# Performance work log

Measured on AMD Instinct MI355X. Metric: run time of the kernel, lower is better.

The kernel has to match this reference:

```python
import jax, jax.numpy as jnp
import numpy as np

B, N, ND, ED = 4, 24, 13, 12          # batch, num_nodes, node feat dim, edge feat dim
H, NH, HD = 256, 8, 32                # hidden, heads, head dim (H == NH*HD)
L, T = 64, 1000                       # transformer layers, max_timestep
_SCALE = 1.0 / float(np.sqrt(H))      # torch divides by sqrt(node_dim)=sqrt(256)


def _ln(x, g, b):
    m = x.mean(-1, keepdims=True)
    v = ((x - m) ** 2).mean(-1, keepdims=True)
    return (x - m) / jnp.sqrt(v + 1e-5) * g + b


def setup_inputs() -> dict:
    key = jax.random.key(0)
    it = iter(jax.random.split(key, 40))
    def w(*s):
        return (jax.random.normal(next(it), s) * 0.02).astype(jnp.float32)
    z = lambda *s: jnp.zeros(s, jnp.float32)
    o = lambda *s: jnp.ones(s, jnp.float32)
    d = {}
    d['nodes'] = jax.random.normal(next(it), (B, N, ND), jnp.float32)
    d['edges'] = jax.random.normal(next(it), (B, N, N, ED), jnp.float32)
    d['conds'] = jax.random.randint(next(it), (B,), 0, T)
    # input MLPs
    d['inN_w1'] = w(ND, H); d['inN_b1'] = z(H); d['inN_w2'] = w(H, H); d['inN_b2'] = z(H)
    d['inE_w1'] = w(ED, H); d['inE_b1'] = z(H); d['inE_w2'] = w(H, H); d['inE_b2'] = z(H)
    d['inC_w1'] = w(T, H);  d['inC_b1'] = z(H); d['inC_w2'] = w(H, H); d['inC_b2'] = z(H)
    # stacked per-layer params (leading dim L, scanned)
    d['qkv_w'] = w(L, H, 3 * H); d['qkv_b'] = z(L, 3 * H)
    d['no_w'] = w(L, H, H); d['no_b'] = z(L, H)
    d['eo_w'] = w(L, H, H); d['eo_b'] = z(L, H)
    d['ln1n_g'] = o(L, H); d['ln1n_b'] = z(L, H)
    d['ln1e_g'] = o(L, H); d['ln1e_b'] = z(L, H)
    d['mn_w1'] = w(L, H, 4 * H); d['mn_b1'] = z(L, 4 * H)
    d['mn_w2'] = w(L, 4 * H, H); d['mn_b2'] = z(L, H)
    d['me_w1'] = w(L, H, 4 * H); d['me_b1'] = z(L, 4 * H)
    d['me_w2'] = w(L, 4 * H, H); d['me_b2'] = z(L, H)
    d['ln2n_g'] = o(L, H); d['ln2n_b'] = z(L, H)
    d['ln2e_g'] = o(L, H); d['ln2e_b'] = z(L, H)
    # output MLPs
    d['outN_w1'] = w(H, H); d['outN_b1'] = z(H); d['outN_w2'] = w(H, ND); d['outN_b2'] = z(ND)
    d['outE_w1'] = w(H, H); d['outE_b1'] = z(H); d['outE_w2'] = w(H, ED); d['outE_b2'] = z(ED)
    return d


def _forward(nodes, edges, conds,
             inN_w1, inN_b1, inN_w2, inN_b2, inE_w1, inE_b1, inE_w2, inE_b2,
             inC_w1, inC_b1, inC_w2, inC_b2,
             qkv_w, qkv_b, no_w, no_b, eo_w, eo_b,
             ln1n_g, ln1n_b, ln1e_g, ln1e_b,
             mn_w1, mn_b1, mn_w2, mn_b2, me_w1, me_b1, me_w2, me_b2,
             ln2n_g, ln2n_b, ln2e_g, ln2e_b,
             outN_w1, outN_b1, outN_w2, outN_b2, outE_w1, outE_b1, outE_w2, outE_b2):
    relu = jax.nn.relu
    c = jax.nn.one_hot(conds, T, dtype=nodes.dtype)
    c = relu(relu(c @ inC_w1 + inC_b1) @ inC_w2 + inC_b2)          # (B,H)
    n = relu(relu(nodes @ inN_w1 + inN_b1) @ inN_w2 + inN_b2)      # (B,N,H)
    e = relu(relu(edges @ inE_w1 + inE_b1) @ inE_w2 + inE_b2)      # (B,N,N,H)

    def layer(carry, p):
        n, e = carry
        (qw, qb, nw, nb, ew, eb, g1n, b1n, g1e, b1e,
         w1n, bb1n, w2n, bb2n, w1e, bb1e, w2e, bb2e, g2n, b2n, g2e, b2e) = p
        nc = n + c[:, None, :]
        q, k, v = jnp.split(nc @ qw + qb, 3, axis=-1)
        q = q.reshape(B, N, NH, HD); k = k.reshape(B, N, NH, HD); v = v.reshape(B, N, NH, HD)
        s5 = jnp.einsum('bihd,bjhd->bijhd', q, k) * _SCALE          # (B,N,N,NH,HD)
        ne5 = s5 + e.reshape(B, N, N, NH, HD)                       # edge-biased scores
        attn = jax.nn.softmax(ne5.sum(-1), axis=2)                  # (B,N,N,NH)
        wv = jnp.einsum('bijh,bjhd->bihd', attn, v).reshape(B, N, H)
        an = _ln(wv @ nw + nb + n, g1n, b1n)
        ae = _ln(relu(ne5.reshape(B, N, N, H) @ ew + eb) + e, g1e, b1e)
        n2 = _ln(relu(an @ w1n + bb1n) @ w2n + bb2n + an, g2n, b2n)
        e2 = _ln(relu(ae @ w1e + bb1e) @ w2e + bb2e + ae, g2e, b2e)
        return (n2, e2), None

    stacked = (qkv_w, qkv_b, no_w, no_b, eo_w, eo_b, ln1n_g, ln1n_b, ln1e_g, ln1e_b,
               mn_w1, mn_b1, mn_w2, mn_b2, me_w1, me_b1, me_w2, me_b2,
               ln2n_g, ln2n_b, ln2e_g, ln2e_b)
    (n, e), _ = jax.lax.scan(layer, (n, e), stacked)
    out_n = relu(n @ outN_w1 + outN_b1) @ outN_w2 + outN_b2
    out_e = relu(e @ outE_w1 + outE_b1) @ outE_w2 + outE_b2
    return out_n, out_e


def reference(nodes, edges, conds,
              inN_w1, inN_b1, inN_w2, inN_b2, inE_w1, inE_b1, inE_w2, inE_b2,
              inC_w1, inC_b1, inC_w2, inC_b2,
              qkv_w, qkv_b, no_w, no_b, eo_w, eo_b,
              ln1n_g, ln1n_b, ln1e_g, ln1e_b,
              mn_w1, mn_b1, mn_w2, mn_b2, me_w1, me_b1, me_w2, me_b2,
              ln2n_g, ln2n_b, ln2e_g, ln2e_b,
              outN_w1, outN_b1, outN_w2, outN_b2, outE_w1, outE_b1, outE_w2, outE_b2):
    return _forward(nodes, edges, conds,
                    inN_w1, inN_b1, inN_w2, inN_b2, inE_w1, inE_b1, inE_w2, inE_b2,
                    inC_w1, inC_b1, inC_w2, inC_b2,
                    qkv_w, qkv_b, no_w, no_b, eo_w, eo_b,
                    ln1n_g, ln1n_b, ln1e_g, ln1e_b,
                    mn_w1, mn_b1, mn_w2, mn_b2, me_w1, me_b1, me_w2, me_b2,
                    ln2n_g, ln2n_b, ln2e_g, ln2e_b,
                    outN_w1, outN_b1, outN_w2, outN_b2, outE_w1, outE_b1, outE_w2, outE_b2)
```

## Files before the change

### kernel.cpp

```cpp
#include <hip/hip_runtime.h>

typedef _Float16 half_t;
typedef _Float16 f16x8 __attribute__((ext_vector_type(8)));
typedef _Float16 f16x4 __attribute__((ext_vector_type(4)));
typedef float f32x4 __attribute__((ext_vector_type(4)));

#define BB 4
#define NNODE 24
#define NLAYER 64
#define SCALE_QK 0.0625f

#define WS_C     0
#define WS_N     1024
#define WS_NACC  25600
#define NACC_STRIDE 24576
#define WS_E     74752
#define WS_AE32  664576
#define WS_AE16  1254400
#define WS_AN16  1549312
#define WS_EPART 1561600
#define EPART_SLICE 589824
#define WS_WTF   3920896
#define SLOT_F16 1376256
#define OFF_QKVT 0
#define OFF_NOT  196608
#define OFF_EOT  262144
#define OFF_MN1T 327680
#define OFF_MN2T 589824
#define OFF_ME1T 851968
#define OFF_ME2T 1114112
#define OFF_INE2T  (3*SLOT_F16)
#define OFF_OUTE1T (3*SLOT_F16 + 65536)

struct Params {
  const float *nodes, *edges; const int* conds;
  const float *inN_w1,*inN_b1,*inN_w2,*inN_b2;
  const float *inE_w1,*inE_b1,*inE_w2,*inE_b2;
  const float *inC_w1,*inC_b1,*inC_w2,*inC_b2;
  const float *qkv_w,*qkv_b,*no_w,*no_b,*eo_w,*eo_b;
  const float *ln1n_g,*ln1n_b,*ln1e_g,*ln1e_b;
  const float *mn_w1,*mn_b1,*mn_w2,*mn_b2,*me_w1,*me_b1,*me_w2,*me_b2;
  const float *ln2n_g,*ln2n_b,*ln2e_g,*ln2e_b;
  const float *outN_w1,*outN_b1,*outN_w2,*outN_b2,*outE_w1,*outE_b1,*outE_w2,*outE_b2;
  float* ws; float* out;
};

template<int NT, int KS, int MT, int LDAH>
__device__ __forceinline__ void gemm_rs_acc(const half_t* __restrict__ WT, int ldb,
                                            const char* __restrict__ A,
                                            f32x4 (&acc)[NT][MT]) {
  const int lane = threadIdx.x & 63;
  const int wv = threadIdx.x >> 6;
  const int l15 = lane & 15;
  const int kg = lane >> 4;
  f16x8 b[NT][KS];
#pragma unroll
  for (int nt = 0; nt < NT; ++nt) {
    const int col = (nt * 8 + wv) * 16 + l15;
#pragma unroll
    for (int ks = 0; ks < KS; ++ks)
      b[nt][ks] = *(const f16x8*)(WT + (size_t)col * ldb + ks * 32 + kg * 8);
  }
#pragma unroll
  for (int m = 0; m < MT; ++m) {
    f16x8 a[KS];
    const int row = m * 16 + l15;
#pragma unroll
    for (int ks = 0; ks < KS; ++ks)
      a[ks] = *(const f16x8*)(A + row * (LDAH * 2) + (((ks * 32 + kg * 8) * 2) ^ ((row & 7) << 4)));
#pragma unroll
    for (int ks = 0; ks < KS; ++ks)
#pragma unroll
      for (int nt = 0; nt < NT; ++nt)
        acc[nt][m] = __builtin_amdgcn_mfma_f32_16x16x32_f16(a[ks], b[nt][ks], acc[nt][m], 0, 0, 0);
  }
}

template<int NT, int KS, int MT, int LDAH, typename EPI>
__device__ __forceinline__ void gemm_rs(const half_t* __restrict__ WT, int ldb,
                                        const char* __restrict__ A, EPI epi) {
  f32x4 acc[NT][MT];
#pragma unroll
  for (int nt = 0; nt < NT; ++nt)
#pragma unroll
    for (int m = 0; m < MT; ++m) {
      f32x4 z = {0.f, 0.f, 0.f, 0.f};
      acc[nt][m] = z;
    }
  gemm_rs_acc<NT, KS, MT, LDAH>(WT, ldb, A, acc);
#pragma unroll
  for (int nt = 0; nt < NT; ++nt)
#pragma unroll
    for (int m = 0; m < MT; ++m)
      epi(nt, m, acc[nt][m]);
}

template<int NTW, int KT, int MT, int LDA, int LDB, typename EPI>
__device__ __forceinline__ void run_gemm_s(const half_t* __restrict__ WT,
                                           const char* __restrict__ A,
                                           EPI epi) {
  const int lane = threadIdx.x & 63;
  const int wv = threadIdx.x >> 6;
  const int l15 = lane & 15;
  const int kg = lane >> 4;
  constexpr int NC = KT / 8;
  constexpr int TC = NC * NTW;
  f16x8 bb[2][8];
  auto ldb = [&](int c, int w) {
    const int kc = c / NTW, n = c % NTW;
    const half_t* bp = WT + (size_t)((n * 8 + wv) * 16 + l15) * LDB + kc * 256 + kg * 8;
#pragma unroll
    for (int q = 0; q < 8; ++q) bb[w][q] = *(const f16x8*)(bp + q * 32);
  };
  f32x4 acc[NTW][MT];
#pragma unroll
  for (int n = 0; n < NTW; ++n)
#pragma unroll
    for (int m = 0; m < MT; ++m) {
      f32x4 z = {0.f, 0.f, 0.f, 0.f};
      acc[n][m] = z;
    }
  ldb(0, 0);
#pragma unroll
  for (int kc = 0; kc < NC; ++kc) {
    f16x8 a[8][MT];
#pragma unroll
    for (int q = 0; q < 8; ++q) {
      const int k0 = (kc * 8 + q) * 32 + kg * 8;
#pragma unroll
      for (int m = 0; m < MT; ++m) {
        const int row = m * 16 + l15;
        a[q][m] = *(const f16x8*)(A + row * (LDA * 2) + ((k0 * 2) ^ ((row & 7) << 4)));
      }
    }
#pragma unroll
    for (int n = 0; n < NTW; ++n) {
      const int c = kc * NTW + n;
      if (c + 1 < TC) ldb(c + 1, (c + 1) & 1);
#pragma unroll
      for (int q = 0; q < 8; ++q)
#pragma unroll
        for (int m = 0; m < MT; ++m)
          acc[n][m] = __builtin_amdgcn_mfma_f32_16x16x32_f16(a[q][m], bb[c & 1][q], acc[n][m], 0, 0, 0);
    }
  }
#pragma unroll
  for (int n = 0; n < NTW; ++n) epi(n, acc[n]);
}

__device__ void conv_matrix_tile(const float* __restrict__ src, half_t* __restrict__ dst,
                                 int K, int Nn, int tk, int tn, char* smem) {
  float* tl = (float*)smem;
  const int t = threadIdx.x;
  const int c = t & 63;
  const int r0 = t >> 6;
  for (int r = r0; r < 64; r += 8)
    tl[r * 65 + c] = src[(size_t)(tk * 64 + r) * Nn + tn * 64 + c];
  __syncthreads();
  for (int r = r0; r < 64; r += 8)
    dst[(size_t)(tn * 64 + r) * K + tk * 64 + c] = (half_t)tl[c * 65 + r];
  __syncthreads();
}

__device__ void conv_layer_tile(const Params& p, half_t* slot, int lw, int tile, char* smem) {
  if (tile < 48)       { conv_matrix_tile(p.qkv_w + (size_t)lw*196608, slot+OFF_QKVT, 256, 768, tile & 3, tile >> 2, smem); }
  else if (tile < 64)  { int t2 = tile-48;  conv_matrix_tile(p.no_w  + (size_t)lw*65536,  slot+OFF_NOT,  256, 256, t2 & 3,  t2 >> 2, smem); }
  else if (tile < 80)  { int t2 = tile-64;  conv_matrix_tile(p.eo_w  + (size_t)lw*65536,  slot+OFF_EOT,  256, 256, t2 & 3,  t2 >> 2, smem); }
  else if (tile < 144) { int t2 = tile-80;  conv_matrix_tile(p.mn_w1 + (size_t)lw*262144, slot+OFF_MN1T, 256, 1024, t2 & 3, t2 >> 2, smem); }
  else if (tile < 208) { int t2 = tile-144; conv_matrix_tile(p.mn_w2 + (size_t)lw*262144, slot+OFF_MN2T, 1024, 256, t2 & 15, t2 >> 4, smem); }
  else if (tile < 272) { int t2 = tile-208; conv_matrix_tile(p.me_w1 + (size_t)lw*262144, slot+OFF_ME1T, 256, 1024, t2 & 3, t2 >> 2, smem); }
  else                 { int t2 = tile-272; conv_matrix_tile(p.me_w2 + (size_t)lw*262144, slot+OFF_ME2T, 1024, 256, t2 & 15, t2 >> 4, smem); }
}

__global__ __launch_bounds__(512, 2) void k_embedA(Params p) {
  __shared__ __align__(16) char smem[17024];
  const int bid = blockIdx.x, tid = threadIdx.x;
  float* ws = p.ws;
  half_t* wt = (half_t*)(ws + WS_WTF);
  if (bid < 4) {
    const int b = bid;
    const int cond = p.conds[b];
    float* t1 = (float*)smem;
    if (tid < 256) t1[tid] = fmaxf(p.inC_w1[(size_t)cond * 256 + tid] + p.inC_b1[tid], 0.f);
    __syncthreads();
    if (tid < 256) {
      float s = p.inC_b2[tid];
      for (int k = 0; k < 256; ++k) s += t1[k] * p.inC_w2[(size_t)k * 256 + tid];
      ws[WS_C + b * 256 + tid] = fmaxf(s, 0.f);
    }
  } else {
    for (int job = bid - 4; job < 704; job += 128) {
      if (job < 336)      conv_layer_tile(p, wt, 0, job, smem);
      else if (job < 672) conv_layer_tile(p, wt + SLOT_F16, 1, job - 336, smem);
      else if (job < 688) { int t2 = job - 672; conv_matrix_tile(p.inE_w2,  wt + OFF_INE2T,  256, 256, t2 & 3, t2 >> 2, smem); }
      else                { int t2 = job - 688; conv_matrix_tile(p.outE_w1, wt + OFF_OUTE1T, 256, 256, t2 & 3, t2 >> 2, smem); }
    }
  }
}

__global__ __launch_bounds__(512, 2) void k_embedB(Params p) {
  __shared__ __align__(16) char smem[24640];
  const int bid = blockIdx.x, tid = threadIdx.x;
  const int lane = tid & 63, wv = tid >> 6, l15 = lane & 15, kg = lane >> 4;
  float* ws = p.ws;
  half_t* wt = (half_t*)(ws + WS_WTF);
  float* e0 = ws + WS_E;
  float* n0 = ws + WS_N;
  if (bid < 96) {
    const int b = bid / NNODE, i = bid % NNODE;
    float* eb = (float*)smem;
    char* t16 = smem + 2048;
    for (int idx = tid; idx < 24 * 12; idx += 512)
      eb[idx] = p.edges[((size_t)(b * NNODE + i) * NNODE + idx / 12) * 12 + idx % 12];
    __syncthreads();
    for (int idx = tid; idx < 32 * 32; idx += 512) {
      int r = idx >> 5, kb = idx & 31, k0 = kb * 8;
      f16x8 v;
#pragma unroll
      for (int j = 0; j < 8; ++j) v[j] = (half_t)0.f;
      if (r < NNODE) {
#pragma unroll
        for (int j = 0; j < 8; ++j) {
          int col = k0 + j;
          float s = p.inE_b1[col];
          for (int kk = 0; kk < 12; ++kk) s += eb[r * 12 + kk] * p.inE_w1[kk * 256 + col];
          v[j] = (half_t)fmaxf(s, 0.f);
        }
      }
      *(f16x8*)(t16 + r * 512 + ((k0 * 2) ^ ((r & 7) << 4))) = v;
    }
    __syncthreads();
    run_gemm_s<2, 8, 2, 256, 256>(wt + OFF_INE2T, t16,
      [&](int n, f32x4 (&accn)[2]) {
        const int col = (n * 8 + wv) * 16 + l15;
        const float bcol = p.inE_b2[col];
#pragma unroll
        for (int m = 0; m < 2; ++m)
#pragma unroll
          for (int r4 = 0; r4 < 4; ++r4) {
            const int row = m * 16 + kg * 4 + r4;
            if (row < NNODE)
              e0[((size_t)(b * NNODE + i) * NNODE + row) * 256 + col] = fmaxf(accn[m][r4] + bcol, 0.f);
          }
      });
  } else {
    const int nb = bid - 96, b = nb >> 1, hf = nb & 1, i0 = hf * 12;
    float* nd = (float*)smem;
    float* t1 = (float*)(smem + 1024);
    for (int idx = tid; idx < 12 * 13; idx += 512)
      nd[(idx / 13) * 16 + (idx % 13)] = p.nodes[(size_t)(b * NNODE + i0 + idx / 13) * 13 + idx % 13];
    __syncthreads();
    for (int idx = tid; idx < 12 * 256; idx += 512) {
      int r = idx >> 8, col = idx & 255;
      float s = p.inN_b1[col];
      for (int kk = 0; kk < 13; ++kk) s += nd[r * 16 + kk] * p.inN_w1[kk * 256 + col];
      t1[r * 257 + col] = fmaxf(s, 0.f);
    }
    __syncthreads();
    {
      int col = tid & 255, rh = tid >> 8;
      float a6[6] = {0.f, 0.f, 0.f, 0.f, 0.f, 0.f};
      for (int k = 0; k < 256; ++k) {
        float w = p.inN_w2[(size_t)k * 256 + col];
#pragma unroll
        for (int r = 0; r < 6; ++r) a6[r] += t1[(rh * 6 + r) * 257 + k] * w;
      }
#pragma unroll
      for (int r = 0; r < 6; ++r) {
        int row = rh * 6 + r;
        n0[(size_t)(b * NNODE + i0 + row) * 256 + col] = fmaxf(a6[r] + p.inN_b2[col], 0.f);
      }
    }
  }
}

__global__ __launch_bounds__(512, 2) void k_attn(Params p, int lyr) {
  __shared__ __align__(16) char smem[139488];
  const int bid = blockIdx.x, tid = threadIdx.x;
  const int lane = tid & 63, wv = tid >> 6, l15 = lane & 15, kg = lane >> 4;
  float* ws = p.ws;
  half_t* wt = (half_t*)(ws + WS_WTF);
  const half_t* slot = wt + (size_t)(lyr % 3) * SLOT_F16;

  if (bid >= 96) {
    if (lyr + 2 < NLAYER) {
      half_t* dslot = wt + (size_t)((lyr + 2) % 3) * SLOT_F16;
      for (int tile = bid - 96; tile < 336; tile += 126)
        conv_layer_tile(p, dslot, lyr + 2, tile, smem);
    }
    return;
  }
  const int b = bid / NNODE, i = bid % NNODE;
  const size_t rowbase = (size_t)(b * NNODE + i) * NNODE;
  char* nc16 = smem;
  half_t* qkv16 = (half_t*)(smem + 16384);
  char* ne5 = smem + 65536;
  float* e32 = (float*)(smem + 81920);
  float* psum = (float*)(smem + 106880);
  float* sc = (float*)(smem + 109952);
  float* wvl = (float*)(smem + 110720);
  float* ni = (float*)(smem + 111744);
  float* anr = (float*)(smem + 112768);
  float* aef = (float*)(smem + 114816);
  float* ae32 = ws + WS_AE32;
  half_t* ae16g = (half_t*)(ws + WS_AE16);
  const half_t* epart = (const half_t*)(ws + WS_EPART);
  const float* nacc_in = ws + WS_NACC + ((lyr + 1) & 1) * NACC_STRIDE;
  float* nacc_out = ws + WS_NACC + (lyr & 1) * NACC_STRIDE;
  const float* cb = ws + WS_C + b * 256;

  for (int r = wv; r < 32; r += 8) {
    const int c = lane * 4;
    f16x4 hv;
    if (r < NNODE) {
      f32x4 y;
      if (lyr == 0) {
        y = *(const f32x4*)(ws + WS_N + (size_t)(b * NNODE + r) * 256 + c);
      } else {
        f32x4 x = *(const f32x4*)(nacc_in + (size_t)(b * NNODE + r) * 256 + c);
        float s = x[0] + x[1] + x[2] + x[3];
        float s2 = x[0]*x[0] + x[1]*x[1] + x[2]*x[2] + x[3]*x[3];
#pragma unroll
        for (int off = 32; off; off >>= 1) { s += __shfl_xor(s, off); s2 += __shfl_xor(s2, off); }
        float mean = s * (1.f / 256.f);
        float rstd = rsqrtf(s2 * (1.f / 256.f) - mean * mean + 1e-5f);
        const float* g = p.ln2n_g + (size_t)(lyr - 1) * 256;
        const float* bv = p.ln2n_b + (size_t)(lyr - 1) * 256;
#pragma unroll
        for (int j = 0; j < 4; ++j) y[j] = (x[j] - mean) * rstd * g[c + j] + bv[c + j];
      }
      if (r == i) *(f32x4*)(ni + c) = y;
#pragma unroll
      for (int j = 0; j < 4; ++j) hv[j] = (half_t)(y[j] + cb[c + j]);
    } else {
#pragma unroll
      for (int j = 0; j < 4; ++j) hv[j] = (half_t)0.f;
    }
    *(f16x4*)(nc16 + r * 512 + ((lane * 8) ^ ((r & 7) << 4))) = hv;
  }
  __syncthreads();
  {
    const float* qb = p.qkv_b + (size_t)lyr * 768;
#pragma unroll
    for (int nn = 0; nn < 3; ++nn) {
      gemm_rs<2, 8, 2, 256>(slot + OFF_QKVT + (size_t)(nn * 256) * 256, 256, nc16,
        [&](int nt, int m, f32x4 v) {
          const int gcol = nn * 256 + (nt * 8 + wv) * 16 + l15;
          const float bc = qb[gcol];
#pragma unroll
          for (int r4 = 0; r4 < 4; ++r4) {
            const int row = m * 16 + kg * 4 + r4;
            qkv16[(size_t)row * 768 + gcol] = (half_t)(v[r4] + bc);
          }
        });
    }
  }
  __syncthreads();
  for (int idx = tid; idx < 32 * 32; idx += 512) {
    int r = idx >> 5, kb = idx & 31, k0 = kb * 8;
    f16x8 v;
#pragma unroll
    for (int j = 0; j < 8; ++j) v[j] = (half_t)0.f;
    if (r < NNODE) {
      const size_t row = rowbase + r;
      float x[8];
      if (lyr == 0) {
        const f32x4 a = *(const f32x4*)(ws + WS_E + row * 256 + k0);
        const f32x4 b4 = *(const f32x4*)(ws + WS_E + row * 256 + k0 + 4);
#pragma unroll
        for (int j = 0; j < 4; ++j) { x[j] = a[j]; x[4 + j] = b4[j]; }
      } else {
        const float* mb2 = p.me_b2 + (size_t)(lyr - 1) * 256;
        const f32x4 a = *(const f32x4*)(ae32 + row * 256 + k0);
        const f32x4 b4 = *(const f32x4*)(ae32 + row * 256 + k0 + 4);
#pragma unroll
        for (int j = 0; j < 4; ++j) { x[j] = a[j] + mb2[k0 + j]; x[4 + j] = b4[j] + mb2[k0 + 4 + j]; }
#pragma unroll
        for (int hb = 0; hb < 8; ++hb) {
          f16x8 pv = *(const f16x8*)(epart + (size_t)hb * EPART_SLICE + row * 256 + k0);
#pragma unroll
          for (int j = 0; j < 8; ++j) x[j] += (float)pv[j];
        }
        float s = 0.f, s2 = 0.f;
#pragma unroll
        for (int j = 0; j < 8; ++j) { s += x[j]; s2 += x[j] * x[j]; }
#pragma unroll
        for (int off = 16; off; off >>= 1) { s += __shfl_xor(s, off); s2 += __shfl_xor(s2, off); }
        float mean = s * (1.f / 256.f);
        float rstd = rsqrtf(s2 * (1.f / 256.f) - mean * mean + 1e-5f);
        const float* g = p.ln2e_g + (size_t)(lyr - 1) * 256;
        const float* bv = p.ln2e_b + (size_t)(lyr - 1) * 256;
#pragma unroll
        for (int j = 0; j < 8; ++j) x[j] = (x[j] - mean) * rstd * g[k0 + j] + bv[k0 + j];
      }
      f16x8 q8 = *(const f16x8*)(qkv16 + (size_t)i * 768 + k0);
      f16x8 k8 = *(const f16x8*)(qkv16 + (size_t)r * 768 + 256 + k0);
      float ps = 0.f;
#pragma unroll
      for (int j = 0; j < 8; ++j) {
        float f = SCALE_QK * (float)q8[j] * (float)k8[j] + x[j];
        v[j] = (half_t)f;
        ps += f;
        e32[r * 260 + k0 + j] = x[j];
      }
      psum[r * 32 + kb] = ps;
    }
    *(f16x8*)(ne5 + r * 512 + ((k0 * 2) ^ ((r & 7) << 4))) = v;
  }
  __syncthreads();
  if (tid < 192) {
    int hq = tid & 7;
    sc[tid] = psum[(tid >> 3) * 32 + hq * 4] + psum[(tid >> 3) * 32 + hq * 4 + 1] +
              psum[(tid >> 3) * 32 + hq * 4 + 2] + psum[(tid >> 3) * 32 + hq * 4 + 3];
  }
  __syncthreads();
  if (tid < 8) {
    const int h = tid;
    float mx = -1e30f;
#pragma unroll
    for (int j = 0; j < 24; ++j) mx = fmaxf(mx, sc[j * 8 + h]);
    float ex[24]; float ssum = 0.f;
#pragma unroll
    for (int j = 0; j < 24; ++j) { ex[j] = __expf(sc[j * 8 + h] - mx); ssum += ex[j]; }
    float inv = 1.f / ssum;
#pragma unroll
    for (int j = 0; j < 24; ++j) sc[j * 8 + h] = ex[j] * inv;
  }
  __syncthreads();
  if (tid < 256) {
    const int d = tid, h = d >> 5;
    float a = 0.f;
#pragma unroll
    for (int j = 0; j < 24; ++j) a += sc[j * 8 + h] * (float)qkv16[(size_t)j * 768 + 512 + d];
    wvl[d] = a;
  }
  {
    const float* eob = p.eo_b + (size_t)lyr * 256;
    gemm_rs<2, 8, 2, 256>(slot + OFF_EOT, 256, ne5,
      [&](int nt, int m, f32x4 v) {
        const int col = (nt * 8 + wv) * 16 + l15;
#pragma unroll
        for (int r4 = 0; r4 < 4; ++r4) {
          const int row = m * 16 + kg * 4 + r4;
          if (row < NNODE)
            aef[row * 257 + col] = fmaxf(v[r4] + eob[col], 0.f) + e32[row * 260 + col];
        }
      });
  }
  __syncthreads();
  {
    const float* g = p.ln1e_g + (size_t)lyr * 256;
    const float* bv = p.ln1e_b + (size_t)lyr * 256;
    for (int r = wv; r < NNODE; r += 8) {
      float x[4];
#pragma unroll
      for (int j = 0; j < 4; ++j) x[j] = aef[r * 257 + lane * 4 + j];
      float s = x[0] + x[1] + x[2] + x[3];
      float s2 = x[0]*x[0] + x[1]*x[1] + x[2]*x[2] + x[3]*x[3];
#pragma unroll
      for (int off = 32; off; off >>= 1) { s += __shfl_xor(s, off); s2 += __shfl_xor(s2, off); }
      float mean = s * (1.f / 256.f);
      float rstd = rsqrtf(s2 * (1.f / 256.f) - mean * mean + 1e-5f);
      f16x4 hv; f32x4 yv;
#pragma unroll
      for (int j = 0; j < 4; ++j) {
        int c = lane * 4 + j;
        float y = (x[j] - mean) * rstd * g[c] + bv[c];
        yv[j] = y; hv[j] = (half_t)y;
      }
      *(f32x4*)(ae32 + (rowbase + r) * 256 + lane * 4) = yv;
      *(f16x4*)(ae16g + (rowbase + r) * 256 + lane * 4) = hv;
    }
  }
  {
    const half_t* NOT_ = slot + OFF_NOT;
    int c = tid & 255, hf = tid >> 8;
    float s = 0.f;
    const half_t* wp = NOT_ + (size_t)c * 256 + hf * 128;
#pragma unroll
    for (int k8 = 0; k8 < 16; ++k8) {
      f16x8 w8 = *(const f16x8*)(wp + k8 * 8);
#pragma unroll
      for (int j = 0; j < 8; ++j) s += wvl[hf * 128 + k8 * 8 + j] * (float)w8[j];
    }
    anr[hf * 256 + c] = s;
  }
  __syncthreads();
  if (wv == 0) {
    const float* nob = p.no_b + (size_t)lyr * 256;
    const float* g = p.ln1n_g + (size_t)lyr * 256;
    const float* bv = p.ln1n_b + (size_t)lyr * 256;
    const float* mb2 = p.mn_b2 + (size_t)lyr * 256;
    float x[4];
#pragma unroll
    for (int j = 0; j < 4; ++j) {
      int c = lane * 4 + j;
      x[j] = anr[c] + anr[256 + c] + nob[c] + ni[c];
    }
    float s = x[0] + x[1] + x[2] + x[3];
    float s2 = x[0]*x[0] + x[1]*x[1] + x[2]*x[2] + x[3]*x[3];
#pragma unroll
    for (int off = 32; off; off >>= 1) { s += __shfl_xor(s, off); s2 += __shfl_xor(s2, off); }
    float mean = s * (1.f / 256.f);
    float rstd = rsqrtf(s2 * (1.f / 256.f) - mean * mean + 1e-5f);
    f16x4 hv; f32x4 av;
#pragma unroll
    for (int j = 0; j < 4; ++j) {
      int c = lane * 4 + j;
      float y = (x[j] - mean) * rstd * g[c] + bv[c];
      hv[j] = (half_t)y;
      av[j] = y + mb2[c];
    }
    *(f16x4*)((half_t*)(ws + WS_AN16) + (size_t)(b * NNODE + i) * 256 + lane * 4) = hv;
    *(f32x4*)(nacc_out + (size_t)(b * NNODE + i) * 256 + lane * 4) = av;
  }
}

__global__ __launch_bounds__(512, 2) void k_mlp(Params p, int lyr) {
  __shared__ __align__(16) char smem[73728];
  const int bid = blockIdx.x, tid = threadIdx.x;
  const int lane = tid & 63, wv = tid >> 6, l15 = lane & 15, kg = lane >> 4;
  float* ws = p.ws;
  half_t* wt = (half_t*)(ws + WS_WTF);
  const half_t* slot = wt + (size_t)(lyr % 3) * SLOT_F16;

  if (bid < 192) {
    const int rb = bid >> 3, hb = bid & 7;
    const int row0 = rb * 96;
    char* A16 = smem;
    char* hl = smem + 49152;
    const half_t* aeg = (const half_t*)(ws + WS_AE16) + (size_t)row0 * 256;
    for (int idx = tid; idx < 96 * 32; idx += 512) {
      int r = idx >> 5, c8 = idx & 31;
      f16x8 v = *(const f16x8*)(aeg + r * 256 + c8 * 8);
      *(f16x8*)(A16 + r * 512 + ((c8 * 16) ^ ((r & 7) << 4))) = v;
    }
    __syncthreads();
    const float* mb1 = p.me_b1 + (size_t)lyr * 1024 + hb * 128;
    gemm_rs<1, 8, 6, 256>(slot + OFF_ME1T + (size_t)(hb * 128) * 256, 256, A16,
      [&](int nt, int m, f32x4 v) {
        const int colb = wv * 16 + l15;
        const float bc = mb1[colb];
#pragma unroll
        for (int r4 = 0; r4 < 4; ++r4) {
          const int row = m * 16 + kg * 4 + r4;
          *(half_t*)(hl + row * 256 + ((colb * 2) ^ ((row & 7) << 4))) = (half_t)fmaxf(v[r4] + bc, 0.f);
        }
      });
    __syncthreads();
    half_t* ep = (half_t*)(ws + WS_EPART) + (size_t)hb * EPART_SLICE + (size_t)row0 * 256;
    gemm_rs<2, 4, 6, 128>(slot + OFF_ME2T + hb * 128, 1024, hl,
      [&](int nt, int m, f32x4 v) {
        const int col = (nt * 8 + wv) * 16 + l15;
#pragma unroll
        for (int r4 = 0; r4 < 4; ++r4)
          ep[(size_t)(m * 16 + kg * 4 + r4) * 256 + col] = (half_t)v[r4];
      });
  } else {
    const int hb = bid - 192;
    char* A16 = smem;
    char* hl = smem + 49152;
    const half_t* ang = (const half_t*)(ws + WS_AN16);
    for (int idx = tid; idx < 96 * 32; idx += 512) {
      int r = idx >> 5, c8 = idx & 31;
      f16x8 v = *(const f16x8*)(ang + (size_t)r * 256 + c8 * 8);
      *(f16x8*)(A16 + r * 512 + ((c8 * 16) ^ ((r & 7) << 4))) = v;
    }
    __syncthreads();
    const float* mb1 = p.mn_b1 + (size_t)lyr * 1024 + hb * 128;
    gemm_rs<1, 8, 6, 256>(slot + OFF_MN1T + (size_t)(hb * 128) * 256, 256, A16,
      [&](int nt, int m, f32x4 v) {
        const int colb = wv * 16 + l15;
        const float bc = mb1[colb];
#pragma unroll
        for (int r4 = 0; r4 < 4; ++r4) {
          const int row = m * 16 + kg * 4 + r4;
          *(half_t*)(hl + row * 256 + ((colb * 2) ^ ((row & 7) << 4))) = (half_t)fmaxf(v[r4] + bc, 0.f);
        }
      });
    __syncthreads();
    float* nacc_out = ws + WS_NACC + (lyr & 1) * NACC_STRIDE;
    gemm_rs<2, 4, 6, 128>(slot + OFF_MN2T + hb * 128, 1024, hl,
      [&](int nt, int m, f32x4 v) {
        const int col = (nt * 8 + wv) * 16 + l15;
#pragma unroll
        for (int r4 = 0; r4 < 4; ++r4)
          atomicAdd(&nacc_out[(size_t)(m * 16 + kg * 4 + r4) * 256 + col], v[r4]);
      });
  }
}

__global__ __launch_bounds__(512, 2) void k_out(Params p) {
  __shared__ __align__(16) char smem[49472];
  const int bid = blockIdx.x, tid = threadIdx.x;
  const int lane = tid & 63, wv = tid >> 6, l15 = lane & 15, kg = lane >> 4;
  float* ws = p.ws;
  half_t* wt = (half_t*)(ws + WS_WTF);
  const float* ae32 = ws + WS_AE32;
  const half_t* epart = (const half_t*)(ws + WS_EPART);
  if (bid < 96) {
    const int b = bid / NNODE, i = bid % NNODE;
    const size_t rowbase = (size_t)(b * NNODE + i) * NNODE;
    char* A16 = smem;
    float* h2f = (float*)(smem + 16384);
    const float* mb2 = p.me_b2 + (size_t)63 * 256;
    const float* g = p.ln2e_g + (size_t)63 * 256;
    const float* bvv = p.ln2e_b + (size_t)63 * 256;
    for (int idx = tid; idx < 32 * 32; idx += 512) {
      int r = idx >> 5, kb = idx & 31, k0 = kb * 8;
      f16x8 v;
#pragma unroll
      for (int j = 0; j < 8; ++j) v[j] = (half_t)0.f;
      if (r < NNODE) {
        const size_t row = rowbase + r;
        float x[8];
        const f32x4 a = *(const f32x4*)(ae32 + row * 256 + k0);
        const f32x4 b4 = *(const f32x4*)(ae32 + row * 256 + k0 + 4);
#pragma unroll
        for (int j = 0; j < 4; ++j) { x[j] = a[j] + mb2[k0 + j]; x[4 + j] = b4[j] + mb2[k0 + 4 + j]; }
#pragma unroll
        for (int hb = 0; hb < 8; ++hb) {
          f16x8 pv = *(const f16x8*)(epart + (size_t)hb * EPART_SLICE + row * 256 + k0);
#pragma unroll
          for (int j = 0; j < 8; ++j) x[j] += (float)pv[j];
        }
        float s = 0.f, s2 = 0.f;
#pragma unroll
        for (int j = 0; j < 8; ++j) { s += x[j]; s2 += x[j] * x[j]; }
#pragma unroll
        for (int off = 16; off; off >>= 1) { s += __shfl_xor(s, off); s2 += __shfl_xor(s2, off); }
        float mean = s * (1.f / 256.f);
        float rstd = rsqrtf(s2 * (1.f / 256.f) - mean * mean + 1e-5f);
#pragma unroll
        for (int j = 0; j < 8; ++j)
          v[j] = (half_t)((x[j] - mean) * rstd * g[k0 + j] + bvv[k0 + j]);
      }
      *(f16x8*)(A16 + r * 512 + ((k0 * 2) ^ ((r & 7) << 4))) = v;
    }
    __syncthreads();
    run_gemm_s<2, 8, 2, 256, 256>(wt + OFF_OUTE1T, A16,
      [&](int n, f32x4 (&accn)[2]) {
        const int col = (n * 8 + wv) * 16 + l15;
#pragma unroll
        for (int m = 0; m < 2; ++m)
#pragma unroll
          for (int r4 = 0; r4 < 4; ++r4) {
            const int row = m * 16 + kg * 4 + r4;
            h2f[row * 257 + col] = (row < NNODE) ? fmaxf(accn[m][r4] + p.outE_b1[col], 0.f) : 0.f;
          }
      });
    __syncthreads();
    for (int pr = tid; pr < 24 * 12; pr += 512) {
      int j = pr / 12, oc = pr % 12;
      float s = p.outE_b2[oc];
      for (int k = 0; k < 256; ++k) s += h2f[j * 257 + k] * p.outE_w2[k * 12 + oc];
      p.out[1248 + ((size_t)(b * NNODE + i) * NNODE + j) * 12 + oc] = s;
    }
  } else {
    const int nb = bid - 96, bq = nb >> 1, hf = nb & 1, i0 = hf * 12;
    float* nl = (float*)smem;
    float* t1f = (float*)(smem + 12544);
    const float* n_acc = ws + WS_NACC + 1 * NACC_STRIDE;
    const float* g = p.ln2n_g + (size_t)63 * 256;
    const float* bvv = p.ln2n_b + (size_t)63 * 256;
    for (int r = wv; r < 12; r += 8) {
      const int row = bq * NNODE + i0 + r;
      const int c = lane * 4;
      f32x4 x = *(const f32x4*)(n_acc + (size_t)row * 256 + c);
      float s = x[0] + x[1] + x[2] + x[3];
      float s2 = x[0]*x[0] + x[1]*x[1] + x[2]*x[2] + x[3]*x[3];
#pragma unroll
      for (int off = 32; off; off >>= 1) { s += __shfl_xor(s, off); s2 += __shfl_xor(s2, off); }
      float mean = s * (1.f / 256.f);
      float rstd = rsqrtf(s2 * (1.f / 256.f) - mean * mean + 1e-5f);
      f32x4 y;
#pragma unroll
      for (int j = 0; j < 4; ++j) y[j] = (x[j] - mean) * rstd * g[c + j] + bvv[c + j];
      *(f32x4*)(nl + r * 257 + c) = y;
    }
    __syncthreads();
    {
      int col = tid & 255, rh = tid >> 8;
      float a6[6] = {0.f, 0.f, 0.f, 0.f, 0.f, 0.f};
      for (int k = 0; k < 256; ++k) {
        float w = p.outN_w1[(size_t)k * 256 + col];
#pragma unroll
        for (int r = 0; r < 6; ++r) a6[r] += nl[(rh * 6 + r) * 257 + k] * w;
      }
#pragma unroll
      for (int r = 0; r < 6; ++r)
        t1f[(rh * 6 + r) * 257 + col] = fmaxf(a6[r] + p.outN_b1[col], 0.f);
    }
    __syncthreads();
    for (int pr = tid; pr < 12 * 13; pr += 512) {
      int il = pr / 13, oc = pr % 13;
      float s = p.outN_b2[oc];
      for (int k = 0; k < 256; ++k) s += t1f[il * 257 + k] * p.outN_w2[k * 13 + oc];
      p.out[((size_t)(bq * NNODE) + i0 + il) * 13 + oc] = s;
    }
  }
}

extern "C" void kernel_launch(void* const* d_in, const int* in_sizes, int n_in,
                              void* d_out, int out_size, void* d_ws, size_t ws_size,
                              hipStream_t stream) {
  (void)in_sizes; (void)n_in; (void)out_size; (void)ws_size;
  Params p;
  const float* const* fi = (const float* const*)d_in;
  p.nodes = fi[0]; p.edges = fi[1]; p.conds = (const int*)d_in[2];
  p.inN_w1 = fi[3]; p.inN_b1 = fi[4]; p.inN_w2 = fi[5]; p.inN_b2 = fi[6];
  p.inE_w1 = fi[7]; p.inE_b1 = fi[8]; p.inE_w2 = fi[9]; p.inE_b2 = fi[10];
  p.inC_w1 = fi[11]; p.inC_b1 = fi[12]; p.inC_w2 = fi[13]; p.inC_b2 = fi[14];
  p.qkv_w = fi[15]; p.qkv_b = fi[16]; p.no_w = fi[17]; p.no_b = fi[18];
  p.eo_w = fi[19]; p.eo_b = fi[20];
  p.ln1n_g = fi[21]; p.ln1n_b = fi[22]; p.ln1e_g = fi[23]; p.ln1e_b = fi[24];
  p.mn_w1 = fi[25]; p.mn_b1 = fi[26]; p.mn_w2 = fi[27]; p.mn_b2 = fi[28];
  p.me_w1 = fi[29]; p.me_b1 = fi[30]; p.me_w2 = fi[31]; p.me_b2 = fi[32];
  p.ln2n_g = fi[33]; p.ln2n_b = fi[34]; p.ln2e_g = fi[35]; p.ln2e_b = fi[36];
  p.outN_w1 = fi[37]; p.outN_b1 = fi[38]; p.outN_w2 = fi[39]; p.outN_b2 = fi[40];
  p.outE_w1 = fi[41]; p.outE_b1 = fi[42]; p.outE_w2 = fi[43]; p.outE_b2 = fi[44];
  p.ws = (float*)d_ws; p.out = (float*)d_out;

  k_embedA<<<dim3(132), dim3(512), 0, stream>>>(p);
  k_embedB<<<dim3(104), dim3(512), 0, stream>>>(p);
  for (int l = 0; l < NLAYER; ++l) {
    k_attn<<<dim3(222), dim3(512), 0, stream>>>(p, l);
    k_mlp<<<dim3(200), dim3(512), 0, stream>>>(p, l);
  }
  k_out<<<dim3(104), dim3(512), 0, stream>>>(p);
}
```

Before: 2.953 ms.

## Prefetch edge inputs and MLP weights into registers, shrink attention LDS footprint

The attention kernel now issues the global loads for the edge residual and the eight MLP partial slices at kernel start, so they overlap the QKV GEMM instead of following it. It stores only the query row and the K/V rows in LDS and reuses the fp32 edge buffer for the output, cutting shared memory from about 139KB to about 91KB so two blocks can fit per CU. In k_mlp the first-GEMM weight fragments are loaded into registers before the activation staging loop, hiding that global latency. The trade-off is higher register pressure from the prefetched values, which could cause spills.

```diff
diff --git a/kernel.cpp b/kernel.cpp
--- a/kernel.cpp
+++ b/kernel.cpp
@@ -95,6 +95,37 @@
       epi(nt, m, acc[nt][m]);
 }
 
+template<int KS>
+__device__ __forceinline__ void load_b1(const half_t* __restrict__ WT, int ldb, f16x8 (&b)[KS]) {
+  const int lane = threadIdx.x & 63, wvq = threadIdx.x >> 6;
+  const int col = wvq * 16 + (lane & 15), kg = lane >> 4;
+#pragma unroll
+  for (int ks = 0; ks < KS; ++ks)
+    b[ks] = *(const f16x8*)(WT + (size_t)col * ldb + ks * 32 + kg * 8);
+}
+
+template<int KS, int MT, int LDAH, typename EPI>
+__device__ __forceinline__ void gemm_rs_preb(const f16x8 (&b)[KS], const char* __restrict__ A, EPI epi) {
+  const int lane = threadIdx.x & 63;
+  const int l15 = lane & 15, kg = lane >> 4;
+  f32x4 acc[MT];
+#pragma unroll
+  for (int m = 0; m < MT; ++m) { f32x4 z = {0.f,0.f,0.f,0.f}; acc[m] = z; }
+#pragma unroll
+  for (int m = 0; m < MT; ++m) {
+    const int row = m * 16 + l15;
+    f16x8 a[KS];
+#pragma unroll
+    for (int ks = 0; ks < KS; ++ks)
+      a[ks] = *(const f16x8*)(A + row * (LDAH * 2) + (((ks * 32 + kg * 8) * 2) ^ ((row & 7) << 4)));
+#pragma unroll
+    for (int ks = 0; ks < KS; ++ks)
+      acc[m] = __builtin_amdgcn_mfma_f32_16x16x32_f16(a[ks], b[ks], acc[m], 0, 0, 0);
+  }
+#pragma unroll
+  for (int m = 0; m < MT; ++m) epi(m, acc[m]);
+}
+
 template<int NTW, int KT, int MT, int LDA, int LDB, typename EPI>
 __device__ __forceinline__ void run_gemm_s(const half_t* __restrict__ WT,
                                            const char* __restrict__ A,
@@ -275,7 +306,7 @@
 }
 
 __global__ __launch_bounds__(512, 2) void k_attn(Params p, int lyr) {
-  __shared__ __align__(16) char smem[139488];
+  __shared__ __align__(16) char smem[90752];
   const int bid = blockIdx.x, tid = threadIdx.x;
   const int lane = tid & 63, wv = tid >> 6, l15 = lane & 15, kg = lane >> 4;
   float* ws = p.ws;
@@ -293,21 +324,52 @@
   const int b = bid / NNODE, i = bid % NNODE;
   const size_t rowbase = (size_t)(b * NNODE + i) * NNODE;
   char* nc16 = smem;
-  half_t* qkv16 = (half_t*)(smem + 16384);
-  char* ne5 = smem + 65536;
-  float* e32 = (float*)(smem + 81920);
-  float* psum = (float*)(smem + 106880);
-  float* sc = (float*)(smem + 109952);
-  float* wvl = (float*)(smem + 110720);
-  float* ni = (float*)(smem + 111744);
-  float* anr = (float*)(smem + 112768);
-  float* aef = (float*)(smem + 114816);
+  half_t* kv16 = (half_t*)(smem + 16384);
+  half_t* qi16 = (half_t*)(smem + 40960);
+  char* ne5 = smem + 41472;
+  float* e32a = (float*)(smem + 57856);
+  float* psum = (float*)(smem + 82816);
+  float* sc = (float*)(smem + 85888);
+  float* wvl = (float*)(smem + 86656);
+  float* ni = (float*)(smem + 87680);
+  float* anr = (float*)(smem + 88704);
   float* ae32 = ws + WS_AE32;
   half_t* ae16g = (half_t*)(ws + WS_AE16);
   const half_t* epart = (const half_t*)(ws + WS_EPART);
   const float* nacc_in = ws + WS_NACC + ((lyr + 1) & 1) * NACC_STRIDE;
   float* nacc_out = ws + WS_NACC + (lyr & 1) * NACC_STRIDE;
   const float* cb = ws + WS_C + b * 256;
+
+  f16x8 pa0[8], pa1[8];
+  f32x4 aa0[2], aa1[2];
+  {
+    const int r0_ = tid >> 5, k00 = (tid & 31) * 8;
+    const size_t row0 = rowbase + r0_;
+    if (lyr == 0) {
+      aa0[0] = *(const f32x4*)(ws + WS_E + row0 * 256 + k00);
+      aa0[1] = *(const f32x4*)(ws + WS_E + row0 * 256 + k00 + 4);
+    } else {
+      aa0[0] = *(const f32x4*)(ae32 + row0 * 256 + k00);
+      aa0[1] = *(const f32x4*)(ae32 + row0 * 256 + k00 + 4);
+#pragma unroll
+      for (int hb = 0; hb < 8; ++hb)
+        pa0[hb] = *(const f16x8*)(epart + (size_t)hb * EPART_SLICE + row0 * 256 + k00);
+    }
+    if (tid < 256) {
+      const int r1_ = 16 + (tid >> 5);
+      const size_t row1 = rowbase + r1_;
+      if (lyr == 0) {
+        aa1[0] = *(const f32x4*)(ws + WS_E + row1 * 256 + k00);
+        aa1[1] = *(const f32x4*)(ws + WS_E + row1 * 256 + k00 + 4);
+      } else {
+        aa1[0] = *(const f32x4*)(ae32 + row1 * 256 + k00);
+        aa1[1] = *(const f32x4*)(ae32 + row1 * 256 + k00 + 4);
+#pragma unroll
+        for (int hb = 0; hb < 8; ++hb)
+          pa1[hb] = *(const f16x8*)(epart + (size_t)hb * EPART_SLICE + row1 * 256 + k00);
+      }
+    }
+  }
 
   for (int r = wv; r < 32; r += 8) {
     const int c = lane * 4;
@@ -341,46 +403,54 @@
   __syncthreads();
   {
     const float* qb = p.qkv_b + (size_t)lyr * 768;
-#pragma unroll
-    for (int nn = 0; nn < 3; ++nn) {
-      gemm_rs<2, 8, 2, 256>(slot + OFF_QKVT + (size_t)(nn * 256) * 256, 256, nc16,
-        [&](int nt, int m, f32x4 v) {
-          const int gcol = nn * 256 + (nt * 8 + wv) * 16 + l15;
-          const float bc = qb[gcol];
-#pragma unroll
-          for (int r4 = 0; r4 < 4; ++r4) {
-            const int row = m * 16 + kg * 4 + r4;
-            qkv16[(size_t)row * 768 + gcol] = (half_t)(v[r4] + bc);
-          }
-        });
-    }
+    gemm_rs<2, 8, 2, 256>(slot + OFF_QKVT, 256, nc16,
+      [&](int nt, int m, f32x4 v) {
+        const int col = (nt * 8 + wv) * 16 + l15;
+        const float bc = qb[col];
+#pragma unroll
+        for (int r4 = 0; r4 < 4; ++r4) {
+          const int row = m * 16 + kg * 4 + r4;
+          if (row == i) qi16[col] = (half_t)(v[r4] + bc);
+        }
+      });
+    gemm_rs<2, 8, 2, 256>(slot + OFF_QKVT + (size_t)256 * 256, 256, nc16,
+      [&](int nt, int m, f32x4 v) {
+        const int col = (nt * 8 + wv) * 16 + l15;
+        const float bc = qb[256 + col];
+#pragma unroll
+        for (int r4 = 0; r4 < 4; ++r4) {
+          const int row = m * 16 + kg * 4 + r4;
+          if (row < NNODE) kv16[(size_t)row * 512 + col] = (half_t)(v[r4] + bc);
+        }
+      });
+    gemm_rs<2, 8, 2, 256>(slot + OFF_QKVT + (size_t)512 * 256, 256, nc16,
+      [&](int nt, int m, f32x4 v) {
+        const int col = (nt * 8 + wv) * 16 + l15;
+        const float bc = qb[512 + col];
+#pragma unroll
+        for (int r4 = 0; r4 < 4; ++r4) {
+          const int row = m * 16 + kg * 4 + r4;
+          if (row < NNODE) kv16[(size_t)row * 512 + 256 + col] = (half_t)(v[r4] + bc);
+        }
+      });
   }
   __syncthreads();
-  for (int idx = tid; idx < 32 * 32; idx += 512) {
-    int r = idx >> 5, kb = idx & 31, k0 = kb * 8;
-    f16x8 v;
-#pragma unroll
-    for (int j = 0; j < 8; ++j) v[j] = (half_t)0.f;
-    if (r < NNODE) {
-      const size_t row = rowbase + r;
+  {
+    const float* gE = (lyr > 0) ? p.ln2e_g + (size_t)(lyr - 1) * 256 : nullptr;
+    const float* bE = (lyr > 0) ? p.ln2e_b + (size_t)(lyr - 1) * 256 : nullptr;
+    const float* mb2 = (lyr > 0) ? p.me_b2 + (size_t)(lyr - 1) * 256 : nullptr;
+    {
+      const int r = tid >> 5, k0 = (tid & 31) * 8;
       float x[8];
-      if (lyr == 0) {
-        const f32x4 a = *(const f32x4*)(ws + WS_E + row * 256 + k0);
-        const f32x4 b4 = *(const f32x4*)(ws + WS_E + row * 256 + k0 + 4);
-#pragma unroll
-        for (int j = 0; j < 4; ++j) { x[j] = a[j]; x[4 + j] = b4[j]; }
-      } else {
-        const float* mb2 = p.me_b2 + (size_t)(lyr - 1) * 256;
-        const f32x4 a = *(const f32x4*)(ae32 + row * 256 + k0);
-        const f32x4 b4 = *(const f32x4*)(ae32 + row * 256 + k0 + 4);
-#pragma unroll
-        for (int j = 0; j < 4; ++j) { x[j] = a[j] + mb2[k0 + j]; x[4 + j] = b4[j] + mb2[k0 + 4 + j]; }
-#pragma unroll
-        for (int hb = 0; hb < 8; ++hb) {
-          f16x8 pv = *(const f16x8*)(epart + (size_t)hb * EPART_SLICE + row * 256 + k0);
-#pragma unroll
-          for (int j = 0; j < 8; ++j) x[j] += (float)pv[j];
-        }
+#pragma unroll
+      for (int j = 0; j < 4; ++j) { x[j] = aa0[0][j]; x[4 + j] = aa0[1][j]; }
+      if (lyr > 0) {
+#pragma unroll
+        for (int j = 0; j < 8; ++j) x[j] += mb2[k0 + j];
+#pragma unroll
+        for (int hb = 0; hb < 8; ++hb)
+#pragma unroll
+          for (int j = 0; j < 8; ++j) x[j] += (float)pa0[hb][j];
         float s = 0.f, s2 = 0.f;
 #pragma unroll
         for (int j = 0; j < 8; ++j) { s += x[j]; s2 += x[j] * x[j]; }
@@ -388,24 +458,67 @@
         for (int off = 16; off; off >>= 1) { s += __shfl_xor(s, off); s2 += __shfl_xor(s2, off); }
         float mean = s * (1.f / 256.f);
         float rstd = rsqrtf(s2 * (1.f / 256.f) - mean * mean + 1e-5f);
-        const float* g = p.ln2e_g + (size_t)(lyr - 1) * 256;
-        const float* bv = p.ln2e_b + (size_t)(lyr - 1) * 256;
-#pragma unroll
-        for (int j = 0; j < 8; ++j) x[j] = (x[j] - mean) * rstd * g[k0 + j] + bv[k0 + j];
-      }
-      f16x8 q8 = *(const f16x8*)(qkv16 + (size_t)i * 768 + k0);
-      f16x8 k8 = *(const f16x8*)(qkv16 + (size_t)r * 768 + 256 + k0);
+#pragma unroll
+        for (int j = 0; j < 8; ++j) x[j] = (x[j] - mean) * rstd * gE[k0 + j] + bE[k0 + j];
+      }
+      f16x8 q8 = *(const f16x8*)(qi16 + k0);
+      f16x8 k8 = *(const f16x8*)(kv16 + (size_t)r * 512 + k0);
+      f16x8 v;
       float ps = 0.f;
 #pragma unroll
       for (int j = 0; j < 8; ++j) {
         float f = SCALE_QK * (float)q8[j] * (float)k8[j] + x[j];
         v[j] = (half_t)f;
         ps += f;
-        e32[r * 260 + k0 + j] = x[j];
-      }
-      psum[r * 32 + kb] = ps;
-    }
-    *(f16x8*)(ne5 + r * 512 + ((k0 * 2) ^ ((r & 7) << 4))) = v;
+        e32a[r * 260 + k0 + j] = x[j];
+      }
+      psum[r * 32 + (tid & 31)] = ps;
+      *(f16x8*)(ne5 + r * 512 + ((k0 * 2) ^ ((r & 7) << 4))) = v;
+    }
+    {
+      const int idx = 512 + tid;
+      const int r = idx >> 5, k0 = (idx & 31) * 8;
+      if (r < NNODE) {
+        float x[8];
+#pragma unroll
+        for (int j = 0; j < 4; ++j) { x[j] = aa1[0][j]; x[4 + j] = aa1[1][j]; }
+        if (lyr > 0) {
+#pragma unroll
+          for (int j = 0; j < 8; ++j) x[j] += mb2[k0 + j];
+#pragma unroll
+          for (int hb = 0; hb < 8; ++hb)
+#pragma unroll
+            for (int j = 0; j < 8; ++j) x[j] += (float)pa1[hb][j];
+          float s = 0.f, s2 = 0.f;
+#pragma unroll
+          for (int j = 0; j < 8; ++j) { s += x[j]; s2 += x[j] * x[j]; }
+#pragma unroll
+          for (int off = 16; off; off >>= 1) { s += __shfl_xor(s, off); s2 += __shfl_xor(s2, off); }
+          float mean = s * (1.f / 256.f);
+          float rstd = rsqrtf(s2 * (1.f / 256.f) - mean * mean + 1e-5f);
+#pragma unroll
+          for (int j = 0; j < 8; ++j) x[j] = (x[j] - mean) * rstd * gE[k0 + j] + bE[k0 + j];
+        }
+        f16x8 q8 = *(const f16x8*)(qi16 + k0);
+        f16x8 k8 = *(const f16x8*)(kv16 + (size_t)r * 512 + k0);
+        f16x8 v;
+        float ps = 0.f;
+#pragma unroll
+        for (int j = 0; j < 8; ++j) {
+          float f = SCALE_QK * (float)q8[j] * (float)k8[j] + x[j];
+          v[j] = (half_t)f;
+          ps += f;
+          e32a[r * 260 + k0 + j] = x[j];
+        }
+        psum[r * 32 + (idx & 31)] = ps;
+        *(f16x8*)(ne5 + r * 512 + ((k0 * 2) ^ ((r & 7) << 4))) = v;
+      } else {
+        f16x8 z;
+#pragma unroll
+        for (int j = 0; j < 8; ++j) z[j] = (half_t)0.f;
+        *(f16x8*)(ne5 + r * 512 + ((k0 * 2) ^ ((r & 7) << 4))) = z;
+      }
+    }
   }
   __syncthreads();
   if (tid < 192) {
@@ -431,7 +544,7 @@
     const int d = tid, h = d >> 5;
     float a = 0.f;
 #pragma unroll
-    for (int j = 0; j < 24; ++j) a += sc[j * 8 + h] * (float)qkv16[(size_t)j * 768 + 512 + d];
+    for (int j = 0; j < 24; ++j) a += sc[j * 8 + h] * (float)kv16[(size_t)j * 512 + 256 + d];
     wvl[d] = a;
   }
   {
@@ -443,7 +556,7 @@
         for (int r4 = 0; r4 < 4; ++r4) {
           const int row = m * 16 + kg * 4 + r4;
           if (row < NNODE)
-            aef[row * 257 + col] = fmaxf(v[r4] + eob[col], 0.f) + e32[row * 260 + col];
+            e32a[row * 260 + col] = fmaxf(v[r4] + eob[col], 0.f) + e32a[row * 260 + col];
         }
       });
   }
@@ -454,7 +567,7 @@
     for (int r = wv; r < NNODE; r += 8) {
       float x[4];
 #pragma unroll
-      for (int j = 0; j < 4; ++j) x[j] = aef[r * 257 + lane * 4 + j];
+      for (int j = 0; j < 4; ++j) x[j] = e32a[r * 260 + lane * 4 + j];
       float s = x[0] + x[1] + x[2] + x[3];
       float s2 = x[0]*x[0] + x[1]*x[1] + x[2]*x[2] + x[3]*x[3];
 #pragma unroll
@@ -529,6 +642,8 @@
     const int row0 = rb * 96;
     char* A16 = smem;
     char* hl = smem + 49152;
+    f16x8 b1[8];
+    load_b1<8>(slot + OFF_ME1T + (size_t)(hb * 128) * 256, 256, b1);
     const half_t* aeg = (const half_t*)(ws + WS_AE16) + (size_t)row0 * 256;
     for (int idx = tid; idx < 96 * 32; idx += 512) {
       int r = idx >> 5, c8 = idx & 31;
@@ -537,8 +652,8 @@
     }
     __syncthreads();
     const float* mb1 = p.me_b1 + (size_t)lyr * 1024 + hb * 128;
-    gemm_rs<1, 8, 6, 256>(slot + OFF_ME1T + (size_t)(hb * 128) * 256, 256, A16,
-      [&](int nt, int m, f32x4 v) {
+    gemm_rs_preb<8, 6, 256>(b1, A16,
+      [&](int m, f32x4 v) {
         const int colb = wv * 16 + l15;
         const float bc = mb1[colb];
 #pragma unroll
@@ -560,6 +675,8 @@
     const int hb = bid - 192;
     char* A16 = smem;
     char* hl = smem + 49152;
+    f16x8 b1[8];
+    load_b1<8>(slot + OFF_MN1T + (size_t)(hb * 128) * 256, 256, b1);
     const half_t* ang = (const half_t*)(ws + WS_AN16);
     for (int idx = tid; idx < 96 * 32; idx += 512) {
       int r = idx >> 5, c8 = idx & 31;
@@ -568,8 +685,8 @@
     }
     __syncthreads();
     const float* mb1 = p.mn_b1 + (size_t)lyr * 1024 + hb * 128;
-    gemm_rs<1, 8, 6, 256>(slot + OFF_MN1T + (size_t)(hb * 128) * 256, 256, A16,
-      [&](int nt, int m, f32x4 v) {
+    gemm_rs_preb<8, 6, 256>(b1, A16,
+      [&](int m, f32x4 v) {
         const int colb = wv * 16 + l15;
         const float bc = mb1[colb];
 #pragma unroll
```

New measurement: 3.060 ms. +3.7%, slower.
